# Kernel optimization log

Measured on AMD Instinct MI355X. Metric: run time of the kernel, lower is better.

Reference implementation:

```python
import math
import jax, jax.numpy as jnp
import numpy as np

HEAD_SIZE = 64
DEPTH = 0

def lambda_init_fn(depth):
    depth = depth + 1
    return 0.8 - 0.6 * math.exp(-0.3 * depth)

def setup_inputs() -> dict:
    key = jax.random.key(0)
    ks = jax.random.split(key, 9)
    B, T, C = 4, 4096, 1024
    H2 = 2 * HEAD_SIZE  # 128
    return {
        "x":  jax.random.normal(ks[0], (B, T, C), dtype=jnp.float32),
        "Wq": jax.random.normal(ks[1], (C, H2), dtype=jnp.float32) * (C ** -0.5),
        "Wk": jax.random.normal(ks[2], (C, H2), dtype=jnp.float32) * (C ** -0.5),
        "Wv": jax.random.normal(ks[3], (C, H2), dtype=jnp.float32) * (C ** -0.5),
        "lambda_q1": jax.random.normal(ks[4], (HEAD_SIZE,), dtype=jnp.float32) * 0.1,
        "lambda_q2": jax.random.normal(ks[5], (HEAD_SIZE,), dtype=jnp.float32) * 0.1,
        "lambda_k1": jax.random.normal(ks[6], (HEAD_SIZE,), dtype=jnp.float32) * 0.1,
        "lambda_k2": jax.random.normal(ks[7], (HEAD_SIZE,), dtype=jnp.float32) * 0.1,
    }

def reference(x, Wq, Wk, Wv, lambda_q1, lambda_q2, lambda_k1, lambda_k2):
    B, T, C = x.shape
    q = x @ Wq  # (B,T,2*hs)
    k = x @ Wk
    v = x @ Wv  # (B,T,2*hs)
    q1, q2 = jnp.split(q, 2, axis=-1)
    k1, k2 = jnp.split(k, 2, axis=-1)
    scale = 1.0 / math.sqrt(HEAD_SIZE)
    w1 = jnp.einsum('btd,bsd->bts', q1, k1) * scale  # (B,T,T)
    w2 = jnp.einsum('btd,bsd->bts', q2, k2) * scale
    causal = jnp.tril(jnp.ones((T, T), dtype=bool))
    neg_inf = jnp.float32(-jnp.inf)
    w1 = jnp.where(causal, w1, neg_inf)
    w2 = jnp.where(causal, w2, neg_inf)
    lam1 = jnp.exp(jnp.sum(lambda_q1 * lambda_k1))
    lam2 = jnp.exp(jnp.sum(lambda_q2 * lambda_k2))
    lam = lam1 - lam2 + lambda_init_fn(DEPTH)
    weights = jax.nn.softmax(w1, axis=-1) - lam * jax.nn.softmax(w2, axis=-1)
    out = jnp.einsum('bts,bsd->btd', weights, v)  # (B,T,2*hs)
    return out
```

## Files before the change

kernel.cpp:

```cpp
#include <hip/hip_runtime.h>
#include <hip/hip_bf16.h>

typedef __bf16 bf16x8 __attribute__((ext_vector_type(8)));
typedef float f32x4 __attribute__((ext_vector_type(4)));

#define LAMBDA_INIT 0.3555090675909693f
#define CEXP 0.18033688011112042f

#define K_OFF   ((size_t)16384 * 128)
#define VT_OFF  ((size_t)2 * 16384 * 128)
#define PART_OFF_BYTES ((size_t)12582912)
#define REC_FLOATS 4160

__device__ __forceinline__ unsigned short f2bf(float f) {
    __hip_bfloat16 h = __float2bfloat16(f);
    unsigned short u;
    __builtin_memcpy(&u, &h, 2);
    return u;
}
__device__ __forceinline__ float bf2f(unsigned short u) {
    unsigned int x = ((unsigned int)u) << 16;
    float f;
    __builtin_memcpy(&f, &x, 4);
    return f;
}
__device__ __forceinline__ unsigned int cvt_pk_bf16(float a, float b) {
    unsigned int r;
    asm volatile("v_cvt_pk_bf16_f32 %0, %1, %2" : "=v"(r) : "v"(a), "v"(b));
    return r;
}

__global__ __launch_bounds__(256) void prep_wt(
    const float* __restrict__ Wq, const float* __restrict__ Wk,
    const float* __restrict__ Wv, unsigned short* __restrict__ WT) {
    const int kt = blockIdx.x, nt = blockIdx.y, mat = blockIdx.z;
    const float* W = (mat == 0) ? Wq : (mat == 1) ? Wk : Wv;
    unsigned short* O = WT + (size_t)mat * 128 * 1024;
    __shared__ float tb[64][65];
    const int r = threadIdx.x >> 2, c4 = (threadIdx.x & 3) * 16;
    for (int j = 0; j < 4; ++j) {
        float4 v = *(const float4*)&W[(size_t)(kt * 64 + r) * 128 + nt * 64 + c4 + j * 4];
        tb[r][c4 + j * 4 + 0] = v.x;
        tb[r][c4 + j * 4 + 1] = v.y;
        tb[r][c4 + j * 4 + 2] = v.z;
        tb[r][c4 + j * 4 + 3] = v.w;
    }
    __syncthreads();
    unsigned short tmp[16];
    for (int j = 0; j < 16; ++j) tmp[j] = f2bf(tb[c4 + j][r]);
    *(uint4*)&O[(size_t)(nt * 64 + r) * 1024 + kt * 64 + c4] = *(uint4*)&tmp[0];
    *(uint4*)&O[(size_t)(nt * 64 + r) * 1024 + kt * 64 + c4 + 8] = *(uint4*)&tmp[8];
}

__global__ __launch_bounds__(512) void qkv_fused(
    const float* __restrict__ x, const unsigned short* __restrict__ WT,
    unsigned short* __restrict__ qkv) {
    const int tid = threadIdx.x;
    const int l = tid & 63, w = tid >> 6;
    const int g = l >> 4, i16 = l & 15;
    const int rh = w >> 2, cp = w & 3;
    const int row0 = blockIdx.x * 64;

    __shared__ unsigned short xs[64][72];
    __shared__ unsigned short wt[384][72];

    f32x4 acc[2][6];
    const f32x4 z4 = {0.f, 0.f, 0.f, 0.f};
    for (int rt = 0; rt < 2; ++rt)
        for (int ct = 0; ct < 6; ++ct) acc[rt][ct] = z4;

    const int xrow = tid >> 3, xcol = (tid & 7) * 8;
    const int wn = tid >> 3, wk8 = (tid & 7) * 8;
    const float* xp = &x[(size_t)(row0 + xrow) * 1024 + xcol];
    const unsigned short* wp = &WT[(size_t)wn * 1024 + wk8];

    float4 ax0, ax1, bx0, bx1;
    uint4 aw0, aw1, aw2, aw3, aw4, aw5, bw0, bw1, bw2, bw3, bw4, bw5;

#define QI(k0_, X0, X1, W0, W1, W2, W3, W4, W5) do {                        \
        X0 = *(const float4*)&xp[(k0_)];                                    \
        X1 = *(const float4*)&xp[(k0_) + 4];                                \
        W0 = *(const uint4*)&wp[(k0_)];                                     \
        W1 = *(const uint4*)&wp[64 * 1024 + (k0_)];                         \
        W2 = *(const uint4*)&wp[128 * 1024 + (k0_)];                        \
        W3 = *(const uint4*)&wp[192 * 1024 + (k0_)];                        \
        W4 = *(const uint4*)&wp[256 * 1024 + (k0_)];                        \
        W5 = *(const uint4*)&wp[320 * 1024 + (k0_)];                        \
    } while (0)

#define QS(X0, X1, W0, W1, W2, W3, W4, W5) do {                             \
        *(ushort4*)&xs[xrow][xcol]     = make_ushort4(f2bf(X0.x), f2bf(X0.y), f2bf(X0.z), f2bf(X0.w)); \
        *(ushort4*)&xs[xrow][xcol + 4] = make_ushort4(f2bf(X1.x), f2bf(X1.y), f2bf(X1.z), f2bf(X1.w)); \
        *(uint4*)&wt[wn +   0][wk8] = W0;                                   \
        *(uint4*)&wt[wn +  64][wk8] = W1;                                   \
        *(uint4*)&wt[wn + 128][wk8] = W2;                                   \
        *(uint4*)&wt[wn + 192][wk8] = W3;                                   \
        *(uint4*)&wt[wn + 256][wk8] = W4;                                   \
        *(uint4*)&wt[wn + 320][wk8] = W5;                                   \
    } while (0)

#define QMFMA() do {                                                        \
        bf16x8 af[2][2];                                                    \
        _Pragma("unroll")                                                   \
        for (int rt = 0; rt < 2; ++rt)                                      \
            for (int cc = 0; cc < 2; ++cc)                                  \
                af[rt][cc] = *(const bf16x8*)&xs[rh * 32 + rt * 16 + i16][cc * 32 + 8 * g]; \
        _Pragma("unroll")                                                   \
        for (int ct = 0; ct < 6; ++ct) {                                    \
            _Pragma("unroll")                                               \
            for (int cc = 0; cc < 2; ++cc) {                                \
                bf16x8 bb = *(const bf16x8*)&wt[cp * 96 + ct * 16 + i16][cc * 32 + 8 * g]; \
                for (int rt = 0; rt < 2; ++rt)                              \
                    acc[rt][ct] = __builtin_amdgcn_mfma_f32_16x16x32_bf16(af[rt][cc], bb, acc[rt][ct], 0, 0, 0); \
            }                                                               \
        }                                                                   \
    } while (0)

    QI(0, ax0, ax1, aw0, aw1, aw2, aw3, aw4, aw5);
    QI(64, bx0, bx1, bw0, bw1, bw2, bw3, bw4, bw5);
    #pragma unroll 1
    for (int k0 = 0; k0 < 1024; k0 += 128) {
        __syncthreads();
        QS(ax0, ax1, aw0, aw1, aw2, aw3, aw4, aw5);
        if (k0 + 128 < 1024) QI(k0 + 128, ax0, ax1, aw0, aw1, aw2, aw3, aw4, aw5);
        __syncthreads();
        QMFMA();
        __syncthreads();
        QS(bx0, bx1, bw0, bw1, bw2, bw3, bw4, bw5);
        if (k0 + 192 < 1024) QI(k0 + 192, bx0, bx1, bw0, bw1, bw2, bw3, bw4, bw5);
        __syncthreads();
        QMFMA();
    }
#undef QI
#undef QS
#undef QMFMA

    __syncthreads();
    unsigned short(*ts)[392] = (unsigned short(*)[392]) & wt[0][0];
    #pragma unroll
    for (int rt = 0; rt < 2; ++rt)
        for (int ct = 0; ct < 6; ++ct) {
            const float sc = (cp * 96 + ct * 16 < 128) ? CEXP : 1.0f;
            for (int r = 0; r < 4; ++r)
                ts[rh * 32 + rt * 16 + g * 4 + r][cp * 96 + ct * 16 + i16] = f2bf(acc[rt][ct][r] * sc);
        }
    __syncthreads();

    const int bq = row0 >> 12;
    const int s = (row0 >> 6) & 63;
    {
        unsigned short* outp = qkv + (size_t)row0 * 128;
        #pragma unroll
        for (int it = 0; it < 2; ++it) {
            int tr = it * 32 + (tid >> 4), dv0 = (tid & 15) * 8;
            *(uint4*)&outp[tr * 128 + dv0] = *(const uint4*)&ts[tr][dv0];
        }
    }
    {
        unsigned short* kimg = qkv + K_OFF + ((size_t)(bq * 64 + s) * 2) * 4096;
        #pragma unroll
        for (int it = 0; it < 2; ++it) {
            int lin = it * 512 + tid;
            int branch_ = (lin >> 9) & 1;
            int region = (lin >> 6) & 7;
            int slot = lin & 63;
            int row = (region >> 1) * 16 + (slot & 15);
            int d = 128 + branch_ * 64 + (region & 1) * 32 + (slot >> 4) * 8;
            uint4 vv = *(const uint4*)&ts[row][d];
            *(uint4*)&kimg[(size_t)branch_ * 4096 + (region * 64 + slot) * 8] = vv;
        }
    }
    {
        unsigned short* vimg = qkv + VT_OFF + (size_t)(bq * 64 + s) * 8192;
        #pragma unroll
        for (int it = 0; it < 2; ++it) {
            int lin = it * 512 + tid;
            int region = (lin >> 6) & 15;
            int slot = lin & 63;
            int dv = 256 + (region >> 1) * 16 + (slot & 15);
            int kv0 = (region & 1) * 32 + (slot >> 4) * 8;
            unsigned short tmp[8];
            #pragma unroll
            for (int e = 0; e < 8; ++e) tmp[e] = ts[kv0 + e][dv];
            *(uint4*)&vimg[(region * 64 + slot) * 8] = *(uint4*)tmp;
        }
    }
}

__global__ __launch_bounds__(256, 3) void diff_attn_pair(
    const unsigned short* __restrict__ q, const unsigned short* __restrict__ kimg,
    const unsigned short* __restrict__ vimg,
    float* __restrict__ part, int ncs) {
    const int bx = blockIdx.x, b = blockIdx.y;
    const int c = blockIdx.z >> 1, branch = blockIdx.z & 1;
    const int bxe = (c & 1) ? (31 - bx) : bx;
    const int t_o = 63 - 2 * bxe, t_e = t_o - 1;
    const int n = t_o + 1;
    const int s_lo = (c * n) >> ncs, smax = ((c + 1) * n) >> ncs;

    if (s_lo >= smax) return;

    const int tid = threadIdx.x;
    const int l = tid & 63, w = tid >> 6;
    const int gq = l >> 4, i16 = l & 15;
    const float NEGINF = -__builtin_inff();

    __shared__ unsigned short ksf[2][4096];
    __shared__ unsigned short psf[8192];

    float* recA = part + ((((size_t)(b * 64 + t_e) << ncs) + c) * 2 + branch) * REC_FLOATS;
    float* recB = part + ((((size_t)(b * 64 + t_o) << ncs) + c) * 2 + branch) * REC_FLOATS;
    const bool emptyA = (s_lo > t_e);

    const size_t bbase = (size_t)b * 4096;
    const unsigned short* kimg_b = kimg + (size_t)b * 524288;
    const unsigned short* vimg_b = vimg + (size_t)b * 524288;
    const int tid8 = tid * 8;
    const int l8 = l * 8;
    const f32x4 z4 = {0.f, 0.f, 0.f, 0.f};

    bf16x8 qfA[2], qfB[2];
    #pragma unroll
    for (int cc = 0; cc < 2; ++cc) {
        qfA[cc] = *(const bf16x8*)&q[(bbase + t_e * 64 + w * 16 + i16) * 128 + branch * 64 + cc * 32 + 8 * gq];
        qfB[cc] = *(const bf16x8*)&q[(bbase + t_o * 64 + w * 16 + i16) * 128 + branch * 64 + cc * 32 + 8 * gq];
    }

    float lsumA = 0.f, lsumB = 0.f;
    f32x4 acc[2][4][2];
    for (int qs = 0; qs < 2; ++qs)
        for (int qg = 0; qg < 4; ++qg)
            for (int j = 0; j < 2; ++j) acc[qs][qg][j] = z4;

    int pdst[4];
    #pragma unroll
    for (int cb = 0; cb < 4; ++cb)
        pdst[cb] = ((w * 2 + (cb >> 1)) * 64 + ((cb & 1) * 2 + (gq >> 1)) * 16 + i16) * 8 + (gq & 1) * 4;

    uint4 kr0, kr1;
    bf16x8 vb00, vb01, vb10, vb11;

#define K_ISSUE(s_) do {                                                            \
        const unsigned short* kp = &kimg_b[((size_t)(s_) * 2 + branch) * 4096];     \
        kr0 = *(const uint4*)&kp[tid8];                                             \
        kr1 = *(const uint4*)&kp[tid8 + 2048];                                      \
    } while (0)
#define V_ISSUE(s_) do {                                                            \
        const unsigned short* vp = &vimg_b[(size_t)(s_) * 8192 + w * 2048];         \
        vb00 = *(const bf16x8*)&vp[l8];                                             \
        vb01 = *(const bf16x8*)&vp[512 + l8];                                       \
        vb10 = *(const bf16x8*)&vp[1024 + l8];                                      \
        vb11 = *(const bf16x8*)&vp[1536 + l8];                                      \
    } while (0)

    K_ISSUE(s_lo);
    V_ISSUE(s_lo);
    int pb = 0;
    #pragma unroll 1
    for (int s = s_lo; s < smax; ++s) {
        *(uint4*)&ksf[pb][tid8] = kr0;
        *(uint4*)&ksf[pb][tid8 + 2048] = kr1;
        if (s + 1 < smax) K_ISSUE(s + 1);
        __syncthreads();
        const bool aAct = (s != t_o);

        f32x4 scA[4], scB[4];
        for (int cb = 0; cb < 4; ++cb) { scA[cb] = z4; scB[cb] = z4; }
        __builtin_amdgcn_s_setprio(1);
        #pragma unroll
        for (int cb = 0; cb < 4; ++cb)
            for (int cc = 0; cc < 2; ++cc) {
                bf16x8 kf = *(const bf16x8*)&ksf[pb][((cb * 2 + cc) * 64 + l) * 8];
                scA[cb] = __builtin_amdgcn_mfma_f32_16x16x32_bf16(kf, qfA[cc], scA[cb], 0, 0, 0);
                scB[cb] = __builtin_amdgcn_mfma_f32_16x16x32_bf16(kf, qfB[cc], scB[cb], 0, 0, 0);
            }
        __builtin_amdgcn_s_setprio(0);

        if (aAct) {
            if (s == t_e) {
                int ql = w * 16 + i16;
                for (int cb = 0; cb < 4; ++cb)
                    for (int r = 0; r < 4; ++r)
                        if (cb * 16 + gq * 4 + r > ql) scA[cb][r] = NEGINF;
            }
            #pragma unroll
            for (int cb = 0; cb < 4; ++cb) {
                float p0 = exp2f(scA[cb][0]);
                float p1 = exp2f(scA[cb][1]);
                float p2 = exp2f(scA[cb][2]);
                float p3 = exp2f(scA[cb][3]);
                lsumA += (p0 + p1) + (p2 + p3);
                uint2 pw;
                pw.x = cvt_pk_bf16(p0, p1);
                pw.y = cvt_pk_bf16(p2, p3);
                *(uint2*)&psf[pdst[cb]] = pw;
            }
        }
        {
            if (s == t_o) {
                int ql = w * 16 + i16;
                for (int cb = 0; cb < 4; ++cb)
                    for (int r = 0; r < 4; ++r)
                        if (cb * 16 + gq * 4 + r > ql) scB[cb][r] = NEGINF;
            }
            #pragma unroll
            for (int cb = 0; cb < 4; ++cb) {
                float p0 = exp2f(scB[cb][0]);
                float p1 = exp2f(scB[cb][1]);
                float p2 = exp2f(scB[cb][2]);
                float p3 = exp2f(scB[cb][3]);
                lsumB += (p0 + p1) + (p2 + p3);
                uint2 pw;
                pw.x = cvt_pk_bf16(p0, p1);
                pw.y = cvt_pk_bf16(p2, p3);
                *(uint2*)&psf[4096 + pdst[cb]] = pw;
            }
        }
        __syncthreads();

        __builtin_amdgcn_s_setprio(1);
        if (aAct) {
            #pragma unroll
            for (int qg = 0; qg < 4; ++qg) {
                bf16x8 pa0 = *(const bf16x8*)&psf[(qg * 2 + 0) * 512 + l8];
                bf16x8 pa1 = *(const bf16x8*)&psf[(qg * 2 + 1) * 512 + l8];
                acc[0][qg][0] = __builtin_amdgcn_mfma_f32_16x16x32_bf16(pa0, vb00, acc[0][qg][0], 0, 0, 0);
                acc[0][qg][0] = __builtin_amdgcn_mfma_f32_16x16x32_bf16(pa1, vb01, acc[0][qg][0], 0, 0, 0);
                acc[0][qg][1] = __builtin_amdgcn_mfma_f32_16x16x32_bf16(pa0, vb10, acc[0][qg][1], 0, 0, 0);
                acc[0][qg][1] = __builtin_amdgcn_mfma_f32_16x16x32_bf16(pa1, vb11, acc[0][qg][1], 0, 0, 0);
            }
        }
        #pragma unroll
        for (int qg = 0; qg < 4; ++qg) {
            bf16x8 pa0 = *(const bf16x8*)&psf[4096 + (qg * 2 + 0) * 512 + l8];
            bf16x8 pa1 = *(const bf16x8*)&psf[4096 + (qg * 2 + 1) * 512 + l8];
            acc[1][qg][0] = __builtin_amdgcn_mfma_f32_16x16x32_bf16(pa0, vb00, acc[1][qg][0], 0, 0, 0);
            acc[1][qg][0] = __builtin_amdgcn_mfma_f32_16x16x32_bf16(pa1, vb01, acc[1][qg][0], 0, 0, 0);
            acc[1][qg][1] = __builtin_amdgcn_mfma_f32_16x16x32_bf16(pa0, vb10, acc[1][qg][1], 0, 0, 0);
            acc[1][qg][1] = __builtin_amdgcn_mfma_f32_16x16x32_bf16(pa1, vb11, acc[1][qg][1], 0, 0, 0);
        }
        __builtin_amdgcn_s_setprio(0);
        if (s + 1 < smax) V_ISSUE(s + 1);
        pb ^= 1;
    }
#undef K_ISSUE
#undef V_ISSUE

    lsumA += __shfl_xor(lsumA, 16);
    lsumA += __shfl_xor(lsumA, 32);
    lsumB += __shfl_xor(lsumB, 16);
    lsumB += __shfl_xor(lsumB, 32);
    if (!emptyA) {
        if (gq == 0) recA[w * 16 + i16] = lsumA;
        unsigned short* OA = (unsigned short*)(recA + 64);
        for (int qg = 0; qg < 4; ++qg)
            for (int j = 0; j < 2; ++j)
                for (int r = 0; r < 4; ++r)
                    OA[(qg * 16 + gq * 4 + r) * 128 + (w * 2 + j) * 16 + i16] = f2bf(acc[0][qg][j][r]);
    }
    {
        if (gq == 0) recB[w * 16 + i16] = lsumB;
        unsigned short* OB = (unsigned short*)(recB + 64);
        for (int qg = 0; qg < 4; ++qg)
            for (int j = 0; j < 2; ++j)
                for (int r = 0; r < 4; ++r)
                    OB[(qg * 16 + gq * 4 + r) * 128 + (w * 2 + j) * 16 + i16] = f2bf(acc[1][qg][j][r]);
    }
}

__global__ __launch_bounds__(256) void diff_combine(
    const float* __restrict__ part,
    const float* __restrict__ lq1, const float* __restrict__ lq2,
    const float* __restrict__ lk1, const float* __restrict__ lk2,
    float* __restrict__ out, int ncs) {
    const int t = blockIdx.x, b = blockIdx.y;
    const int tid = threadIdx.x;
    const int nc = 1 << ncs;
    const int n = (t | 1) + 1;
    __shared__ float sl[2][64];
    __shared__ float s_lam;

    const float* recbase = part + (((size_t)(b * 64 + t) << ncs)) * 2 * REC_FLOATS;

    if (tid < 64) {
        float s1 = lq1[tid] * lk1[tid];
        float s2 = lq2[tid] * lk2[tid];
        for (int off = 32; off > 0; off >>= 1) {
            s1 += __shfl_xor(s1, off);
            s2 += __shfl_xor(s2, off);
        }
        if (tid == 0) s_lam = expf(s1) - expf(s2) + LAMBDA_INIT;
    }
    if (tid < 128) {
        int r = tid & 63, br = tid >> 6;
        float acc = 0.f;
        for (int c = 0; c < nc; ++c) {
            int lo = (c * n) >> ncs, hi = ((c + 1) * n) >> ncs;
            if (lo >= hi || lo > t) continue;
            acc += recbase[(c * 2 + br) * REC_FLOATS + r];
        }
        sl[br][r] = acc;
    }
    __syncthreads();
    const float lam = s_lam;

    float* op = out + ((size_t)b * 4096 + (size_t)t * 64) * 128;
    for (int grp = 0; grp < 4; ++grp) {
        int gid = grp * 256 + tid;
        int e = gid * 8;
        int row = e >> 7;
        float o1[8] = {0, 0, 0, 0, 0, 0, 0, 0}, o2[8] = {0, 0, 0, 0, 0, 0, 0, 0};
        for (int c = 0; c < nc; ++c) {
            int lo = (c * n) >> ncs, hi = ((c + 1) * n) >> ncs;
            if (lo >= hi || lo > t) continue;
            const unsigned short* O0 = (const unsigned short*)(recbase + (c * 2 + 0) * REC_FLOATS + 64);
            const unsigned short* O1 = (const unsigned short*)(recbase + (c * 2 + 1) * REC_FLOATS + 64);
            uint4 u0 = *(const uint4*)&O0[e];
            uint4 u1 = *(const uint4*)&O1[e];
            const unsigned short* e0 = (const unsigned short*)&u0;
            const unsigned short* e1 = (const unsigned short*)&u1;
            #pragma unroll
            for (int j = 0; j < 8; ++j) {
                o1[j] += bf2f(e0[j]);
                o2[j] += bf2f(e1[j]);
            }
        }
        float l1inv = 1.0f / sl[0][row], l2inv = 1.0f / sl[1][row];
        float res[8];
        #pragma unroll
        for (int j = 0; j < 8; ++j) res[j] = o1[j] * l1inv - lam * o2[j] * l2inv;
        *(float4*)&op[e] = *(float4*)&res[0];
        *(float4*)&op[e + 4] = *(float4*)&res[4];
    }
}

extern "C" void kernel_launch(void* const* d_in, const int* in_sizes, int n_in,
                              void* d_out, int out_size, void* d_ws, size_t ws_size,
                              hipStream_t stream) {
    const float* x   = (const float*)d_in[0];
    const float* Wq  = (const float*)d_in[1];
    const float* Wk  = (const float*)d_in[2];
    const float* Wv  = (const float*)d_in[3];
    const float* lq1 = (const float*)d_in[4];
    const float* lq2 = (const float*)d_in[5];
    const float* lk1 = (const float*)d_in[6];
    const float* lk2 = (const float*)d_in[7];
    float* out = (float*)d_out;
    unsigned short* qkv = (unsigned short*)d_ws;

    const int ncs = 2;
    const size_t part_bytes = (size_t)256 * (1 << ncs) * 2 * REC_FLOATS * 4;
    float* part = (float*)((char*)d_ws + PART_OFF_BYTES);
    unsigned short* WT = (unsigned short*)((char*)d_ws + PART_OFF_BYTES + part_bytes);

    prep_wt<<<dim3(16, 2, 3), 256, 0, stream>>>(Wq, Wk, Wv, WT);
    qkv_fused<<<256, 512, 0, stream>>>(x, WT, qkv);

    const unsigned short* qb = qkv;
    const unsigned short* kb = qkv + K_OFF;
    const unsigned short* vtb = qkv + VT_OFF;
    diff_attn_pair<<<dim3(32, 4, 2 << ncs), 256, 0, stream>>>(qb, kb, vtb, part, ncs);
    diff_combine<<<dim3(64, 4), 256, 0, stream>>>(part, lq1, lq2, lk1, lk2, out, ncs);
}
```

Before: 92.89 us.

## Split QKV projection across two column halves and software-pipeline PV behind QK

The QKV projection kernel now launches a second grid dimension so each block computes half of the 384 output columns, with smaller shared buffers and accumulators and a single-stage prefetch. The aim is more blocks in flight and better occupancy, at the cost of each block re-reading its x tile. In the attention kernel the P buffer is double-buffered, and the P·V MFMAs for step s-1 are issued after the barrier of step s, next to the QK MFMAs. This drops one barrier per iteration and overlaps PV with the score and softmax work. V loads are now issued per step rather than one step ahead, which may expose more load latency.

```diff
diff --git a/kernel.cpp b/kernel.cpp
--- a/kernel.cpp
+++ b/kernel.cpp
@@ -60,129 +60,116 @@
     const int g = l >> 4, i16 = l & 15;
     const int rh = w >> 2, cp = w & 3;
     const int row0 = blockIdx.x * 64;
+    const int np = blockIdx.y;
+    const unsigned short* Wt = WT + (size_t)np * 192 * 1024;
 
     __shared__ unsigned short xs[64][72];
-    __shared__ unsigned short wt[384][72];
-
-    f32x4 acc[2][6];
+    __shared__ unsigned short wt[192][72];
+
+    f32x4 acc[2][3];
     const f32x4 z4 = {0.f, 0.f, 0.f, 0.f};
     for (int rt = 0; rt < 2; ++rt)
-        for (int ct = 0; ct < 6; ++ct) acc[rt][ct] = z4;
+        for (int ct = 0; ct < 3; ++ct) acc[rt][ct] = z4;
 
     const int xrow = tid >> 3, xcol = (tid & 7) * 8;
     const int wn = tid >> 3, wk8 = (tid & 7) * 8;
     const float* xp = &x[(size_t)(row0 + xrow) * 1024 + xcol];
-    const unsigned short* wp = &WT[(size_t)wn * 1024 + wk8];
-
-    float4 ax0, ax1, bx0, bx1;
-    uint4 aw0, aw1, aw2, aw3, aw4, aw5, bw0, bw1, bw2, bw3, bw4, bw5;
-
-#define QI(k0_, X0, X1, W0, W1, W2, W3, W4, W5) do {                        \
-        X0 = *(const float4*)&xp[(k0_)];                                    \
-        X1 = *(const float4*)&xp[(k0_) + 4];                                \
-        W0 = *(const uint4*)&wp[(k0_)];                                     \
-        W1 = *(const uint4*)&wp[64 * 1024 + (k0_)];                         \
-        W2 = *(const uint4*)&wp[128 * 1024 + (k0_)];                        \
-        W3 = *(const uint4*)&wp[192 * 1024 + (k0_)];                        \
-        W4 = *(const uint4*)&wp[256 * 1024 + (k0_)];                        \
-        W5 = *(const uint4*)&wp[320 * 1024 + (k0_)];                        \
+    const unsigned short* wp = &Wt[(size_t)wn * 1024 + wk8];
+
+    float4 ax0, ax1;
+    uint4 aw0, aw1, aw2;
+
+#define QI(k0_) do {                                                        \
+        ax0 = *(const float4*)&xp[(k0_)];                                   \
+        ax1 = *(const float4*)&xp[(k0_) + 4];                               \
+        aw0 = *(const uint4*)&wp[(k0_)];                                    \
+        aw1 = *(const uint4*)&wp[64 * 1024 + (k0_)];                        \
+        aw2 = *(const uint4*)&wp[128 * 1024 + (k0_)];                       \
     } while (0)
 
-#define QS(X0, X1, W0, W1, W2, W3, W4, W5) do {                             \
-        *(ushort4*)&xs[xrow][xcol]     = make_ushort4(f2bf(X0.x), f2bf(X0.y), f2bf(X0.z), f2bf(X0.w)); \
-        *(ushort4*)&xs[xrow][xcol + 4] = make_ushort4(f2bf(X1.x), f2bf(X1.y), f2bf(X1.z), f2bf(X1.w)); \
-        *(uint4*)&wt[wn +   0][wk8] = W0;                                   \
-        *(uint4*)&wt[wn +  64][wk8] = W1;                                   \
-        *(uint4*)&wt[wn + 128][wk8] = W2;                                   \
-        *(uint4*)&wt[wn + 192][wk8] = W3;                                   \
-        *(uint4*)&wt[wn + 256][wk8] = W4;                                   \
-        *(uint4*)&wt[wn + 320][wk8] = W5;                                   \
+#define QS() do {                                                           \
+        *(ushort4*)&xs[xrow][xcol]     = make_ushort4(f2bf(ax0.x), f2bf(ax0.y), f2bf(ax0.z), f2bf(ax0.w)); \
+        *(ushort4*)&xs[xrow][xcol + 4] = make_ushort4(f2bf(ax1.x), f2bf(ax1.y), f2bf(ax1.z), f2bf(ax1.w)); \
+        *(uint4*)&wt[wn +   0][wk8] = aw0;                                  \
+        *(uint4*)&wt[wn +  64][wk8] = aw1;                                  \
+        *(uint4*)&wt[wn + 128][wk8] = aw2;                                  \
     } while (0)
 
-#define QMFMA() do {                                                        \
-        bf16x8 af[2][2];                                                    \
-        _Pragma("unroll")                                                   \
-        for (int rt = 0; rt < 2; ++rt)                                      \
-            for (int cc = 0; cc < 2; ++cc)                                  \
-                af[rt][cc] = *(const bf16x8*)&xs[rh * 32 + rt * 16 + i16][cc * 32 + 8 * g]; \
-        _Pragma("unroll")                                                   \
-        for (int ct = 0; ct < 6; ++ct) {                                    \
-            _Pragma("unroll")                                               \
-            for (int cc = 0; cc < 2; ++cc) {                                \
-                bf16x8 bb = *(const bf16x8*)&wt[cp * 96 + ct * 16 + i16][cc * 32 + 8 * g]; \
-                for (int rt = 0; rt < 2; ++rt)                              \
-                    acc[rt][ct] = __builtin_amdgcn_mfma_f32_16x16x32_bf16(af[rt][cc], bb, acc[rt][ct], 0, 0, 0); \
-            }                                                               \
-        }                                                                   \
-    } while (0)
-
-    QI(0, ax0, ax1, aw0, aw1, aw2, aw3, aw4, aw5);
-    QI(64, bx0, bx1, bw0, bw1, bw2, bw3, bw4, bw5);
+    QI(0);
     #pragma unroll 1
-    for (int k0 = 0; k0 < 1024; k0 += 128) {
+    for (int k0 = 0; k0 < 1024; k0 += 64) {
         __syncthreads();
-        QS(ax0, ax1, aw0, aw1, aw2, aw3, aw4, aw5);
-        if (k0 + 128 < 1024) QI(k0 + 128, ax0, ax1, aw0, aw1, aw2, aw3, aw4, aw5);
+        QS();
+        if (k0 + 64 < 1024) QI(k0 + 64);
         __syncthreads();
-        QMFMA();
-        __syncthreads();
-        QS(bx0, bx1, bw0, bw1, bw2, bw3, bw4, bw5);
-        if (k0 + 192 < 1024) QI(k0 + 192, bx0, bx1, bw0, bw1, bw2, bw3, bw4, bw5);
-        __syncthreads();
-        QMFMA();
+        bf16x8 af[2][2];
+        #pragma unroll
+        for (int rt = 0; rt < 2; ++rt)
+            for (int cc = 0; cc < 2; ++cc)
+                af[rt][cc] = *(const bf16x8*)&xs[rh * 32 + rt * 16 + i16][cc * 32 + 8 * g];
+        #pragma unroll
+        for (int ct = 0; ct < 3; ++ct)
+            for (int cc = 0; cc < 2; ++cc) {
+                bf16x8 bb = *(const bf16x8*)&wt[cp * 48 + ct * 16 + i16][cc * 32 + 8 * g];
+                for (int rt = 0; rt < 2; ++rt)
+                    acc[rt][ct] = __builtin_amdgcn_mfma_f32_16x16x32_bf16(af[rt][cc], bb, acc[rt][ct], 0, 0, 0);
+            }
     }
 #undef QI
 #undef QS
-#undef QMFMA
 
     __syncthreads();
-    unsigned short(*ts)[392] = (unsigned short(*)[392]) & wt[0][0];
+    unsigned short(*ts)[200] = (unsigned short(*)[200]) & wt[0][0];
     #pragma unroll
     for (int rt = 0; rt < 2; ++rt)
-        for (int ct = 0; ct < 6; ++ct) {
-            const float sc = (cp * 96 + ct * 16 < 128) ? CEXP : 1.0f;
+        for (int ct = 0; ct < 3; ++ct) {
+            const float sc = (np == 0 && cp * 48 + ct * 16 < 128) ? CEXP : 1.0f;
             for (int r = 0; r < 4; ++r)
-                ts[rh * 32 + rt * 16 + g * 4 + r][cp * 96 + ct * 16 + i16] = f2bf(acc[rt][ct][r] * sc);
+                ts[rh * 32 + rt * 16 + g * 4 + r][cp * 48 + ct * 16 + i16] = f2bf(acc[rt][ct][r] * sc);
         }
     __syncthreads();
 
     const int bq = row0 >> 12;
     const int s = (row0 >> 6) & 63;
-    {
-        unsigned short* outp = qkv + (size_t)row0 * 128;
-        #pragma unroll
-        for (int it = 0; it < 2; ++it) {
-            int tr = it * 32 + (tid >> 4), dv0 = (tid & 15) * 8;
-            *(uint4*)&outp[tr * 128 + dv0] = *(const uint4*)&ts[tr][dv0];
-        }
-    }
-    {
-        unsigned short* kimg = qkv + K_OFF + ((size_t)(bq * 64 + s) * 2) * 4096;
-        #pragma unroll
-        for (int it = 0; it < 2; ++it) {
-            int lin = it * 512 + tid;
-            int branch_ = (lin >> 9) & 1;
-            int region = (lin >> 6) & 7;
-            int slot = lin & 63;
+    if (np == 0) {
+        {
+            unsigned short* outp = qkv + (size_t)row0 * 128;
+            #pragma unroll
+            for (int it = 0; it < 2; ++it) {
+                int tr = it * 32 + (tid >> 4), dv0 = (tid & 15) * 8;
+                *(uint4*)&outp[tr * 128 + dv0] = *(const uint4*)&ts[tr][dv0];
+            }
+        }
+        {
+            unsigned short* kimg = qkv + K_OFF + ((size_t)(bq * 64 + s) * 2) * 4096;
+            int region = tid >> 6, slot = tid & 63;
             int row = (region >> 1) * 16 + (slot & 15);
-            int d = 128 + branch_ * 64 + (region & 1) * 32 + (slot >> 4) * 8;
+            int d = 128 + (region & 1) * 32 + (slot >> 4) * 8;
             uint4 vv = *(const uint4*)&ts[row][d];
-            *(uint4*)&kimg[(size_t)branch_ * 4096 + (region * 64 + slot) * 8] = vv;
-        }
-    }
-    {
-        unsigned short* vimg = qkv + VT_OFF + (size_t)(bq * 64 + s) * 8192;
-        #pragma unroll
-        for (int it = 0; it < 2; ++it) {
-            int lin = it * 512 + tid;
-            int region = (lin >> 6) & 15;
-            int slot = lin & 63;
-            int dv = 256 + (region >> 1) * 16 + (slot & 15);
-            int kv0 = (region & 1) * 32 + (slot >> 4) * 8;
-            unsigned short tmp[8];
+            *(uint4*)&kimg[(region * 64 + slot) * 8] = vv;
+        }
+    } else {
+        {
+            unsigned short* kimg = qkv + K_OFF + ((size_t)(bq * 64 + s) * 2 + 1) * 4096;
+            int region = tid >> 6, slot = tid & 63;
+            int row = (region >> 1) * 16 + (slot & 15);
+            int d = (region & 1) * 32 + (slot >> 4) * 8;
+            uint4 vv = *(const uint4*)&ts[row][d];
+            *(uint4*)&kimg[(region * 64 + slot) * 8] = vv;
+        }
+        {
+            unsigned short* vimg = qkv + VT_OFF + (size_t)(bq * 64 + s) * 8192;
             #pragma unroll
-            for (int e = 0; e < 8; ++e) tmp[e] = ts[kv0 + e][dv];
-            *(uint4*)&vimg[(region * 64 + slot) * 8] = *(uint4*)tmp;
+            for (int it = 0; it < 2; ++it) {
+                int lin = it * 512 + tid;
+                int region = lin >> 6, slot = lin & 63;
+                int dv = 64 + (region >> 1) * 16 + (slot & 15);
+                int kv0 = (region & 1) * 32 + (slot >> 4) * 8;
+                unsigned short tmp[8];
+                #pragma unroll
+                for (int e = 0; e < 8; ++e) tmp[e] = ts[kv0 + e][dv];
+                *(uint4*)&vimg[(region * 64 + slot) * 8] = *(uint4*)tmp;
+            }
         }
     }
 }
@@ -206,7 +193,7 @@
     const float NEGINF = -__builtin_inff();
 
     __shared__ unsigned short ksf[2][4096];
-    __shared__ unsigned short psf[8192];
+    __shared__ unsigned short psf[2][8192];
 
     float* recA = part + ((((size_t)(b * 64 + t_e) << ncs) + c) * 2 + branch) * REC_FLOATS;
     float* recB = part + ((((size_t)(b * 64 + t_o) << ncs) + c) * 2 + branch) * REC_FLOATS;
@@ -253,29 +240,53 @@
         vb11 = *(const bf16x8*)&vp[1536 + l8];                                      \
     } while (0)
 
+#define PV_CLUSTER(pp_, aPrev_) do {                                                \
+        if (aPrev_) {                                                               \
+            _Pragma("unroll")                                                       \
+            for (int qg = 0; qg < 4; ++qg) {                                        \
+                bf16x8 pa0 = *(const bf16x8*)&psf[pp_][(qg * 2 + 0) * 512 + l8];    \
+                bf16x8 pa1 = *(const bf16x8*)&psf[pp_][(qg * 2 + 1) * 512 + l8];    \
+                acc[0][qg][0] = __builtin_amdgcn_mfma_f32_16x16x32_bf16(pa0, vb00, acc[0][qg][0], 0, 0, 0); \
+                acc[0][qg][0] = __builtin_amdgcn_mfma_f32_16x16x32_bf16(pa1, vb01, acc[0][qg][0], 0, 0, 0); \
+                acc[0][qg][1] = __builtin_amdgcn_mfma_f32_16x16x32_bf16(pa0, vb10, acc[0][qg][1], 0, 0, 0); \
+                acc[0][qg][1] = __builtin_amdgcn_mfma_f32_16x16x32_bf16(pa1, vb11, acc[0][qg][1], 0, 0, 0); \
+            }                                                                       \
+        }                                                                           \
+        _Pragma("unroll")                                                           \
+        for (int qg = 0; qg < 4; ++qg) {                                            \
+            bf16x8 pa0 = *(const bf16x8*)&psf[pp_][4096 + (qg * 2 + 0) * 512 + l8]; \
+            bf16x8 pa1 = *(const bf16x8*)&psf[pp_][4096 + (qg * 2 + 1) * 512 + l8]; \
+            acc[1][qg][0] = __builtin_amdgcn_mfma_f32_16x16x32_bf16(pa0, vb00, acc[1][qg][0], 0, 0, 0); \
+            acc[1][qg][0] = __builtin_amdgcn_mfma_f32_16x16x32_bf16(pa1, vb01, acc[1][qg][0], 0, 0, 0); \
+            acc[1][qg][1] = __builtin_amdgcn_mfma_f32_16x16x32_bf16(pa0, vb10, acc[1][qg][1], 0, 0, 0); \
+            acc[1][qg][1] = __builtin_amdgcn_mfma_f32_16x16x32_bf16(pa1, vb11, acc[1][qg][1], 0, 0, 0); \
+        }                                                                           \
+    } while (0)
+
     K_ISSUE(s_lo);
-    V_ISSUE(s_lo);
-    int pb = 0;
     #pragma unroll 1
     for (int s = s_lo; s < smax; ++s) {
-        *(uint4*)&ksf[pb][tid8] = kr0;
-        *(uint4*)&ksf[pb][tid8 + 2048] = kr1;
+        const int kb = s & 1;
+        *(uint4*)&ksf[kb][tid8] = kr0;
+        *(uint4*)&ksf[kb][tid8 + 2048] = kr1;
         if (s + 1 < smax) K_ISSUE(s + 1);
         __syncthreads();
-        const bool aAct = (s != t_o);
-
+
+        __builtin_amdgcn_s_setprio(1);
+        if (s > s_lo) PV_CLUSTER((s - 1) & 1, (s - 1) != t_o);
         f32x4 scA[4], scB[4];
         for (int cb = 0; cb < 4; ++cb) { scA[cb] = z4; scB[cb] = z4; }
-        __builtin_amdgcn_s_setprio(1);
         #pragma unroll
         for (int cb = 0; cb < 4; ++cb)
             for (int cc = 0; cc < 2; ++cc) {
-                bf16x8 kf = *(const bf16x8*)&ksf[pb][((cb * 2 + cc) * 64 + l) * 8];
+                bf16x8 kf = *(const bf16x8*)&ksf[kb][((cb * 2 + cc) * 64 + l) * 8];
                 scA[cb] = __builtin_amdgcn_mfma_f32_16x16x32_bf16(kf, qfA[cc], scA[cb], 0, 0, 0);
                 scB[cb] = __builtin_amdgcn_mfma_f32_16x16x32_bf16(kf, qfB[cc], scB[cb], 0, 0, 0);
             }
         __builtin_amdgcn_s_setprio(0);
-
+        V_ISSUE(s);
+
+        const bool aAct = (s != t_o);
         if (aAct) {
             if (s == t_e) {
                 int ql = w * 16 + i16;
@@ -293,7 +304,7 @@
                 uint2 pw;
                 pw.x = cvt_pk_bf16(p0, p1);
                 pw.y = cvt_pk_bf16(p2, p3);
-                *(uint2*)&psf[pdst[cb]] = pw;
+                *(uint2*)&psf[kb][pdst[cb]] = pw;
             }
         }
         {
@@ -313,38 +324,18 @@
                 uint2 pw;
                 pw.x = cvt_pk_bf16(p0, p1);
                 pw.y = cvt_pk_bf16(p2, p3);
-                *(uint2*)&psf[4096 + pdst[cb]] = pw;
-            }
-        }
-        __syncthreads();
-
-        __builtin_amdgcn_s_setprio(1);
-        if (aAct) {
-            #pragma unroll
-            for (int qg = 0; qg < 4; ++qg) {
-                bf16x8 pa0 = *(const bf16x8*)&psf[(qg * 2 + 0) * 512 + l8];
-                bf16x8 pa1 = *(const bf16x8*)&psf[(qg * 2 + 1) * 512 + l8];
-                acc[0][qg][0] = __builtin_amdgcn_mfma_f32_16x16x32_bf16(pa0, vb00, acc[0][qg][0], 0, 0, 0);
-                acc[0][qg][0] = __builtin_amdgcn_mfma_f32_16x16x32_bf16(pa1, vb01, acc[0][qg][0], 0, 0, 0);
-                acc[0][qg][1] = __builtin_amdgcn_mfma_f32_16x16x32_bf16(pa0, vb10, acc[0][qg][1], 0, 0, 0);
-                acc[0][qg][1] = __builtin_amdgcn_mfma_f32_16x16x32_bf16(pa1, vb11, acc[0][qg][1], 0, 0, 0);
-            }
-        }
-        #pragma unroll
-        for (int qg = 0; qg < 4; ++qg) {
-            bf16x8 pa0 = *(const bf16x8*)&psf[4096 + (qg * 2 + 0) * 512 + l8];
-            bf16x8 pa1 = *(const bf16x8*)&psf[4096 + (qg * 2 + 1) * 512 + l8];
-            acc[1][qg][0] = __builtin_amdgcn_mfma_f32_16x16x32_bf16(pa0, vb00, acc[1][qg][0], 0, 0, 0);
-            acc[1][qg][0] = __builtin_amdgcn_mfma_f32_16x16x32_bf16(pa1, vb01, acc[1][qg][0], 0, 0, 0);
-            acc[1][qg][1] = __builtin_amdgcn_mfma_f32_16x16x32_bf16(pa0, vb10, acc[1][qg][1], 0, 0, 0);
-            acc[1][qg][1] = __builtin_amdgcn_mfma_f32_16x16x32_bf16(pa1, vb11, acc[1][qg][1], 0, 0, 0);
-        }
-        __builtin_amdgcn_s_setprio(0);
-        if (s + 1 < smax) V_ISSUE(s + 1);
-        pb ^= 1;
-    }
+                *(uint2*)&psf[kb][4096 + pdst[cb]] = pw;
+            }
+        }
+    }
+
+    __syncthreads();
+    __builtin_amdgcn_s_setprio(1);
+    PV_CLUSTER((smax - 1) & 1, (smax - 1) != t_o);
+    __builtin_amdgcn_s_setprio(0);
 #undef K_ISSUE
 #undef V_ISSUE
+#undef PV_CLUSTER
 
     lsumA += __shfl_xor(lsumA, 16);
     lsumA += __shfl_xor(lsumA, 32);
@@ -454,7 +445,7 @@
     unsigned short* WT = (unsigned short*)((char*)d_ws + PART_OFF_BYTES + part_bytes);
 
     prep_wt<<<dim3(16, 2, 3), 256, 0, stream>>>(Wq, Wk, Wv, WT);
-    qkv_fused<<<256, 512, 0, stream>>>(x, WT, qkv);
+    qkv_fused<<<dim3(256, 2), 512, 0, stream>>>(x, WT, qkv);
 
     const unsigned short* qb = qkv;
     const unsigned short* kb = qkv + K_OFF;
```

Result: no change. 91.84 us (-1.1%).
